# Kernel optimization log

Measured on AMD Instinct MI355X. Metric: run time of the kernel, lower is better.

Reference implementation:

```python
import jax, jax.numpy as jnp
import numpy as np

N = 4096
B = 8
NITER = 4

def setup_inputs() -> dict:
    key = jax.random.key(0)
    k1, k2, k3 = jax.random.split(key, 3)
    preds = jax.random.uniform(k1, (B, N), dtype=jnp.float32)
    seed_idx = jax.random.randint(k2, (B, 10), 0, N, dtype=jnp.int64)
    # dense probability matrix (buffer), entries in [0,1)
    prob_matrix = jax.random.uniform(k3, (N, N), dtype=jnp.float32)
    return {"preds": preds, "seed_idx": seed_idx, "prob_matrix": prob_matrix}

def reference(preds, seed_idx, prob_matrix):
    # Original per-row math: new_pred[a] = 1 - prod_b (1 - P[b, a] * pred[b])
    # P2 = P.T * pred.view(1,-1)  =>  P2[a, b] = P[b, a] * pred[b]
    # Vectorized over the batch dim instead of the Python loop.
    # seed_idx is accepted but unused, matching the original forward.
    pred = preds  # [B, N]
    for _ in range(NITER):
        # [B, N(src), N(dst)] intermediate: (1 - pred[b, s] * P[s, d]), prod over s
        pred = 1.0 - jnp.prod(1.0 - pred[:, :, None] * prob_matrix[None, :, :], axis=1)
    return pred
```

## Files before the change

### kernel.cpp

```cpp
#include <hip/hip_runtime.h>

#define NN 4096
#define BB 8
#define SC 32
#define DT 16
#define WAVES 8
#define RPW 16


__global__ void __launch_bounds__(512, 2)
diff_partial_it0(const float* __restrict__ preds,
                 const float* __restrict__ P,
                 unsigned int* __restrict__ P8,
                 float* __restrict__ partial)
{
    const int tid  = threadIdx.x;
    const int lane = tid & 63;
    const int w    = __builtin_amdgcn_readfirstlane(tid >> 6);
    const int d0   = blockIdx.x * 256 + lane * 4;
    const int ch   = blockIdx.y;
    const int row0 = ch * (WAVES * RPW) + w * RPW;

    float4 acc[BB];
#pragma unroll
    for (int b = 0; b < BB; ++b) acc[b] = make_float4(1.f, 1.f, 1.f, 1.f);

    const float* Pp = P + (size_t)row0 * NN + d0;

#pragma unroll
    for (int k = 0; k < RPW; k += 4) {
        float4 pv[4];
#pragma unroll
        for (int j = 0; j < 4; ++j)
            pv[j] = *(const float4*)(Pp + (size_t)(k + j) * NN);

#pragma unroll
        for (int j = 0; j < 4; ++j) {
            const unsigned int e0 = (unsigned int)fmaf(pv[j].x, 255.f, 0.5f);
            const unsigned int e1 = (unsigned int)fmaf(pv[j].y, 255.f, 0.5f);
            const unsigned int e2 = (unsigned int)fmaf(pv[j].z, 255.f, 0.5f);
            const unsigned int e3 = (unsigned int)fmaf(pv[j].w, 255.f, 0.5f);
            P8[((size_t)(row0 + k + j) * NN + d0) >> 2] =
                e0 | (e1 << 8) | (e2 << 16) | (e3 << 24);
        }

#pragma unroll
        for (int j = 0; j < 4; ++j) {
            const int s = row0 + k + j;
#pragma unroll
            for (int b = 0; b < BB; ++b) {
                const float p = preds[b * NN + s];
                acc[b].x *= fmaf(-p, pv[j].x, 1.f);
                acc[b].y *= fmaf(-p, pv[j].y, 1.f);
                acc[b].z *= fmaf(-p, pv[j].z, 1.f);
                acc[b].w *= fmaf(-p, pv[j].w, 1.f);
            }
        }
    }

    __shared__ float4 red[WAVES][BB][64];
#pragma unroll
    for (int b = 0; b < BB; ++b) red[w][b][lane] = acc[b];
    __syncthreads();

    const int b  = tid >> 6;
    const int c4 = tid & 63;
    float4 pr = red[0][b][c4];
#pragma unroll
    for (int w2 = 1; w2 < WAVES; ++w2) {
        const float4 v = red[w2][b][c4];
        pr.x *= v.x; pr.y *= v.y; pr.z *= v.z; pr.w *= v.w;
    }
    *(float4*)(partial + ((size_t)b * SC + ch) * NN + blockIdx.x * 256 + c4 * 4) = pr;
}

__global__ void __launch_bounds__(512, 2)
diff_partial_u8(const float* __restrict__ predT_s,
                const unsigned int* __restrict__ P8,
                float* __restrict__ partial)
{
    const int tid  = threadIdx.x;
    const int lane = tid & 63;
    const int w    = __builtin_amdgcn_readfirstlane(tid >> 6);
    const int d0   = blockIdx.x * 256 + lane * 4;
    const int ch   = blockIdx.y;
    const int row0 = ch * (WAVES * RPW) + w * RPW;

    float4 acc[BB];
#pragma unroll
    for (int b = 0; b < BB; ++b) acc[b] = make_float4(1.f, 1.f, 1.f, 1.f);

    const unsigned int* Pp = P8 + (((size_t)row0 * NN + d0) >> 2);
    const float* pt = predT_s + row0 * BB;

#pragma unroll
    for (int k = 0; k < RPW; k += 4) {
        unsigned int q[4];
#pragma unroll
        for (int j = 0; j < 4; ++j)
            q[j] = Pp[(size_t)(k + j) * (NN / 4)];

#pragma unroll
        for (int j = 0; j < 4; ++j) {
            const float fx = (float)( q[j]        & 0xffu);
            const float fy = (float)((q[j] >> 8)  & 0xffu);
            const float fz = (float)((q[j] >> 16) & 0xffu);
            const float fw = (float)( q[j] >> 24);
#pragma unroll
            for (int b = 0; b < BB; ++b) {
                const float p = pt[(k + j) * BB + b];
                acc[b].x *= fmaf(-p, fx, 1.f);
                acc[b].y *= fmaf(-p, fy, 1.f);
                acc[b].z *= fmaf(-p, fz, 1.f);
                acc[b].w *= fmaf(-p, fw, 1.f);
            }
        }
    }

    __shared__ float4 red[WAVES][BB][64];
#pragma unroll
    for (int b = 0; b < BB; ++b) red[w][b][lane] = acc[b];
    __syncthreads();

    const int b  = tid >> 6;
    const int c4 = tid & 63;
    float4 pr = red[0][b][c4];
#pragma unroll
    for (int w2 = 1; w2 < WAVES; ++w2) {
        const float4 v = red[w2][b][c4];
        pr.x *= v.x; pr.y *= v.y; pr.z *= v.z; pr.w *= v.w;
    }
    *(float4*)(partial + ((size_t)b * SC + ch) * NN + blockIdx.x * 256 + c4 * 4) = pr;
}

__global__ void __launch_bounds__(256)
diff_combine(const float* __restrict__ partial,
             float* __restrict__ predT_next,
             float* __restrict__ out, int write_out)
{
    const int g = blockIdx.x * 256 + threadIdx.x;
    const int b = g >> 12;
    const int d = g & (NN - 1);

    const float* pp = partial + (size_t)b * SC * NN + d;
    float prod = 1.0f;
#pragma unroll
    for (int ch = 0; ch < SC; ++ch)
        prod *= pp[(size_t)ch * NN];

    const float r = 1.0f - prod;
    predT_next[d * BB + b] = r * (1.0f / 255.0f);
    if (write_out) out[g] = r;
}

__global__ void __launch_bounds__(512, 2)
diff_partial_f32(const float* __restrict__ predT,
                 const float* __restrict__ P,
                 float* __restrict__ partial)
{
    const int tid  = threadIdx.x;
    const int lane = tid & 63;
    const int w    = __builtin_amdgcn_readfirstlane(tid >> 6);
    const int d0   = blockIdx.x * 256 + lane * 4;
    const int ch   = blockIdx.y;
    const int row0 = ch * (WAVES * RPW) + w * RPW;

    float4 acc[BB];
#pragma unroll
    for (int b = 0; b < BB; ++b) acc[b] = make_float4(1.f, 1.f, 1.f, 1.f);

    const float* Pp = P + (size_t)row0 * NN + d0;
    const float* pt = predT + row0 * BB;

#pragma unroll
    for (int k = 0; k < RPW; k += 4) {
        float4 pv[4];
#pragma unroll
        for (int j = 0; j < 4; ++j)
            pv[j] = *(const float4*)(Pp + (size_t)(k + j) * NN);
#pragma unroll
        for (int j = 0; j < 4; ++j) {
#pragma unroll
            for (int b = 0; b < BB; ++b) {
                const float p = pt[(k + j) * BB + b];
                acc[b].x *= fmaf(-p, pv[j].x, 1.f);
                acc[b].y *= fmaf(-p, pv[j].y, 1.f);
                acc[b].z *= fmaf(-p, pv[j].z, 1.f);
                acc[b].w *= fmaf(-p, pv[j].w, 1.f);
            }
        }
    }

    __shared__ float4 red[WAVES][BB][64];
#pragma unroll
    for (int b = 0; b < BB; ++b) red[w][b][lane] = acc[b];
    __syncthreads();

    const int b  = tid >> 6;
    const int c4 = tid & 63;
    float4 pr = red[0][b][c4];
#pragma unroll
    for (int w2 = 1; w2 < WAVES; ++w2) {
        const float4 v = red[w2][b][c4];
        pr.x *= v.x; pr.y *= v.y; pr.z *= v.z; pr.w *= v.w;
    }
    *(float4*)(partial + ((size_t)b * SC + ch) * NN + blockIdx.x * 256 + c4 * 4) = pr;
}

__global__ void __launch_bounds__(256)
diff_combine_raw(const float* __restrict__ partial,
                 float* __restrict__ predT_next,
                 float* __restrict__ out, int write_out)
{
    const int g = blockIdx.x * 256 + threadIdx.x;
    const int b = g >> 12;
    const int d = g & (NN - 1);
    const float* pp = partial + (size_t)b * SC * NN + d;
    float prod = 1.0f;
#pragma unroll
    for (int ch = 0; ch < SC; ++ch) prod *= pp[(size_t)ch * NN];
    const float r = 1.0f - prod;
    predT_next[d * BB + b] = r;
    if (write_out) out[g] = r;
}

__global__ void __launch_bounds__(512, 2)
diff_partial_it0_nf(const float* __restrict__ preds,
                    const float* __restrict__ P,
                    float* __restrict__ partial)
{
    const int tid  = threadIdx.x;
    const int lane = tid & 63;
    const int w    = __builtin_amdgcn_readfirstlane(tid >> 6);
    const int d0   = blockIdx.x * 256 + lane * 4;
    const int ch   = blockIdx.y;
    const int row0 = ch * (WAVES * RPW) + w * RPW;

    float4 acc[BB];
#pragma unroll
    for (int b = 0; b < BB; ++b) acc[b] = make_float4(1.f, 1.f, 1.f, 1.f);

    const float* Pp = P + (size_t)row0 * NN + d0;

#pragma unroll
    for (int k = 0; k < RPW; k += 4) {
        float4 pv[4];
#pragma unroll
        for (int j = 0; j < 4; ++j)
            pv[j] = *(const float4*)(Pp + (size_t)(k + j) * NN);
#pragma unroll
        for (int j = 0; j < 4; ++j) {
            const int s = row0 + k + j;
#pragma unroll
            for (int b = 0; b < BB; ++b) {
                const float p = preds[b * NN + s];
                acc[b].x *= fmaf(-p, pv[j].x, 1.f);
                acc[b].y *= fmaf(-p, pv[j].y, 1.f);
                acc[b].z *= fmaf(-p, pv[j].z, 1.f);
                acc[b].w *= fmaf(-p, pv[j].w, 1.f);
            }
        }
    }

    __shared__ float4 red[WAVES][BB][64];
#pragma unroll
    for (int b = 0; b < BB; ++b) red[w][b][lane] = acc[b];
    __syncthreads();

    const int b  = tid >> 6;
    const int c4 = tid & 63;
    float4 pr = red[0][b][c4];
#pragma unroll
    for (int w2 = 1; w2 < WAVES; ++w2) {
        const float4 v = red[w2][b][c4];
        pr.x *= v.x; pr.y *= v.y; pr.z *= v.z; pr.w *= v.w;
    }
    *(float4*)(partial + ((size_t)b * SC + ch) * NN + blockIdx.x * 256 + c4 * 4) = pr;
}

extern "C" void kernel_launch(void* const* d_in, const int* in_sizes, int n_in,
                              void* d_out, int out_size, void* d_ws, size_t ws_size,
                              hipStream_t stream) {
    const float* preds = (const float*)d_in[0];
    const float* P     = (const float*)d_in[2];
    float* out = (float*)d_out;

    char* ws = (char*)d_ws;
    float* partial = (float*)ws;
    float* predT0  = (float*)(ws + (size_t)4 * 1024 * 1024);
    float* predT1  = predT0 + (size_t)NN * BB;
    unsigned int* P8 = (unsigned int*)(ws + (size_t)5 * 1024 * 1024);

    const size_t need_u8 = (size_t)5 * 1024 * 1024 + (size_t)NN * NN;

    dim3 pgrid(DT, SC);
    dim3 cgrid((BB * NN) / 256);
    dim3 block(512);

    if (ws_size >= need_u8) {
        diff_partial_it0<<<pgrid, block, 0, stream>>>(preds, P, P8, partial);
        diff_combine<<<cgrid, 256, 0, stream>>>(partial, predT0, out, 0);
        diff_partial_u8<<<pgrid, block, 0, stream>>>(predT0, P8, partial);
        diff_combine<<<cgrid, 256, 0, stream>>>(partial, predT1, out, 0);
        diff_partial_u8<<<pgrid, block, 0, stream>>>(predT1, P8, partial);
        diff_combine<<<cgrid, 256, 0, stream>>>(partial, predT0, out, 0);
        diff_partial_u8<<<pgrid, block, 0, stream>>>(predT0, P8, partial);
        diff_combine<<<cgrid, 256, 0, stream>>>(partial, predT1, out, 1);
    } else {
        diff_partial_it0_nf<<<pgrid, block, 0, stream>>>(preds, P, partial);
        diff_combine_raw<<<cgrid, 256, 0, stream>>>(partial, predT0, out, 0);
        diff_partial_f32<<<pgrid, block, 0, stream>>>(predT0, P, partial);
        diff_combine_raw<<<cgrid, 256, 0, stream>>>(partial, predT1, out, 0);
        diff_partial_f32<<<pgrid, block, 0, stream>>>(predT1, P, partial);
        diff_combine_raw<<<cgrid, 256, 0, stream>>>(partial, predT0, out, 0);
        diff_partial_f32<<<pgrid, block, 0, stream>>>(predT0, P, partial);
        diff_combine_raw<<<cgrid, 256, 0, stream>>>(partial, predT1, out, 1);
    }
}
```

Before: 56.88 us.

## Fuse combine step into next iteration's partial kernel via per-wave chunk products

Removes the separate combine kernels between iterations. Each wave of the partial kernel now reduces the previous iteration's 32 chunk partials for its own 16 source rows and broadcasts the resulting preds with readlane. The partial buffers are double-buffered, the P8 offset moves to make room, and a final kernel produces the output. This saves three launches and the predT round trip, but every block redundantly recomputes the same row reductions (16 column blocks read the same partial values).

```diff
diff --git a/kernel.cpp b/kernel.cpp
--- a/kernel.cpp
+++ b/kernel.cpp
@@ -74,10 +74,12 @@
     *(float4*)(partial + ((size_t)b * SC + ch) * NN + blockIdx.x * 256 + c4 * 4) = pr;
 }
 
+template <bool U8>
 __global__ void __launch_bounds__(512, 2)
-diff_partial_u8(const float* __restrict__ predT_s,
-                const unsigned int* __restrict__ P8,
-                float* __restrict__ partial)
+diff_fused(const float* __restrict__ prevPartial,
+           const float* __restrict__ Pf,
+           const unsigned int* __restrict__ P8,
+           float* __restrict__ partial)
 {
     const int tid  = threadIdx.x;
     const int lane = tid & 63;
@@ -86,29 +88,55 @@
     const int ch   = blockIdx.y;
     const int row0 = ch * (WAVES * RPW) + w * RPW;
 
+    const int bsel = lane & 7;
+    const int q2   = lane >> 3;
+    const float* qp = prevPartial + (size_t)bsel * SC * NN + row0 + 2 * q2;
+    float prod0 = 1.f, prod1 = 1.f;
+#pragma unroll 8
+    for (int c = 0; c < SC; ++c) {
+        const float2 v = *(const float2*)(qp + (size_t)c * NN);
+        prod0 *= v.x;
+        prod1 *= v.y;
+    }
+    const float sc  = U8 ? (1.f / 255.f) : 1.f;
+    const float pv0 = (1.f - prod0) * sc;
+    const float pv1 = (1.f - prod1) * sc;
+
     float4 acc[BB];
 #pragma unroll
     for (int b = 0; b < BB; ++b) acc[b] = make_float4(1.f, 1.f, 1.f, 1.f);
 
-    const unsigned int* Pp = P8 + (((size_t)row0 * NN + d0) >> 2);
-    const float* pt = predT_s + row0 * BB;
+    const unsigned int* Pp8 = U8 ? P8 + (((size_t)row0 * NN + d0) >> 2) : nullptr;
+    const float*        Ppf = U8 ? nullptr : Pf + (size_t)row0 * NN + d0;
 
 #pragma unroll
     for (int k = 0; k < RPW; k += 4) {
         unsigned int q[4];
-#pragma unroll
-        for (int j = 0; j < 4; ++j)
-            q[j] = Pp[(size_t)(k + j) * (NN / 4)];
-
-#pragma unroll
-        for (int j = 0; j < 4; ++j) {
-            const float fx = (float)( q[j]        & 0xffu);
-            const float fy = (float)((q[j] >> 8)  & 0xffu);
-            const float fz = (float)((q[j] >> 16) & 0xffu);
-            const float fw = (float)( q[j] >> 24);
+        float4 pvf[4];
+#pragma unroll
+        for (int j = 0; j < 4; ++j) {
+            if (U8) q[j]   = Pp8[(size_t)(k + j) * (NN / 4)];
+            else    pvf[j] = *(const float4*)(Ppf + (size_t)(k + j) * NN);
+        }
+
+#pragma unroll
+        for (int j = 0; j < 4; ++j) {
+            const int r = k + j;
+            float fx, fy, fz, fw;
+            if (U8) {
+                fx = (float)( q[j]        & 0xffu);
+                fy = (float)((q[j] >> 8)  & 0xffu);
+                fz = (float)((q[j] >> 16) & 0xffu);
+                fw = (float)( q[j] >> 24);
+            } else {
+                fx = pvf[j].x; fy = pvf[j].y; fz = pvf[j].z; fw = pvf[j].w;
+            }
 #pragma unroll
             for (int b = 0; b < BB; ++b) {
-                const float p = pt[(k + j) * BB + b];
+                const unsigned int pu = ((r & 1) == 0)
+                    ? __builtin_amdgcn_readlane(__float_as_uint(pv0), (r >> 1) * 8 + b)
+                    : __builtin_amdgcn_readlane(__float_as_uint(pv1), (r >> 1) * 8 + b);
+                const float p = __uint_as_float(pu);
                 acc[b].x *= fmaf(-p, fx, 1.f);
                 acc[b].y *= fmaf(-p, fy, 1.f);
                 acc[b].z *= fmaf(-p, fz, 1.f);
@@ -133,30 +161,10 @@
     *(float4*)(partial + ((size_t)b * SC + ch) * NN + blockIdx.x * 256 + c4 * 4) = pr;
 }
 
-__global__ void __launch_bounds__(256)
-diff_combine(const float* __restrict__ partial,
-             float* __restrict__ predT_next,
-             float* __restrict__ out, int write_out)
-{
-    const int g = blockIdx.x * 256 + threadIdx.x;
-    const int b = g >> 12;
-    const int d = g & (NN - 1);
-
-    const float* pp = partial + (size_t)b * SC * NN + d;
-    float prod = 1.0f;
-#pragma unroll
-    for (int ch = 0; ch < SC; ++ch)
-        prod *= pp[(size_t)ch * NN];
-
-    const float r = 1.0f - prod;
-    predT_next[d * BB + b] = r * (1.0f / 255.0f);
-    if (write_out) out[g] = r;
-}
-
 __global__ void __launch_bounds__(512, 2)
-diff_partial_f32(const float* __restrict__ predT,
-                 const float* __restrict__ P,
-                 float* __restrict__ partial)
+diff_partial_it0_nf(const float* __restrict__ preds,
+                    const float* __restrict__ P,
+                    float* __restrict__ partial)
 {
     const int tid  = threadIdx.x;
     const int lane = tid & 63;
@@ -170,77 +178,6 @@
     for (int b = 0; b < BB; ++b) acc[b] = make_float4(1.f, 1.f, 1.f, 1.f);
 
     const float* Pp = P + (size_t)row0 * NN + d0;
-    const float* pt = predT + row0 * BB;
-
-#pragma unroll
-    for (int k = 0; k < RPW; k += 4) {
-        float4 pv[4];
-#pragma unroll
-        for (int j = 0; j < 4; ++j)
-            pv[j] = *(const float4*)(Pp + (size_t)(k + j) * NN);
-#pragma unroll
-        for (int j = 0; j < 4; ++j) {
-#pragma unroll
-            for (int b = 0; b < BB; ++b) {
-                const float p = pt[(k + j) * BB + b];
-                acc[b].x *= fmaf(-p, pv[j].x, 1.f);
-                acc[b].y *= fmaf(-p, pv[j].y, 1.f);
-                acc[b].z *= fmaf(-p, pv[j].z, 1.f);
-                acc[b].w *= fmaf(-p, pv[j].w, 1.f);
-            }
-        }
-    }
-
-    __shared__ float4 red[WAVES][BB][64];
-#pragma unroll
-    for (int b = 0; b < BB; ++b) red[w][b][lane] = acc[b];
-    __syncthreads();
-
-    const int b  = tid >> 6;
-    const int c4 = tid & 63;
-    float4 pr = red[0][b][c4];
-#pragma unroll
-    for (int w2 = 1; w2 < WAVES; ++w2) {
-        const float4 v = red[w2][b][c4];
-        pr.x *= v.x; pr.y *= v.y; pr.z *= v.z; pr.w *= v.w;
-    }
-    *(float4*)(partial + ((size_t)b * SC + ch) * NN + blockIdx.x * 256 + c4 * 4) = pr;
-}
-
-__global__ void __launch_bounds__(256)
-diff_combine_raw(const float* __restrict__ partial,
-                 float* __restrict__ predT_next,
-                 float* __restrict__ out, int write_out)
-{
-    const int g = blockIdx.x * 256 + threadIdx.x;
-    const int b = g >> 12;
-    const int d = g & (NN - 1);
-    const float* pp = partial + (size_t)b * SC * NN + d;
-    float prod = 1.0f;
-#pragma unroll
-    for (int ch = 0; ch < SC; ++ch) prod *= pp[(size_t)ch * NN];
-    const float r = 1.0f - prod;
-    predT_next[d * BB + b] = r;
-    if (write_out) out[g] = r;
-}
-
-__global__ void __launch_bounds__(512, 2)
-diff_partial_it0_nf(const float* __restrict__ preds,
-                    const float* __restrict__ P,
-                    float* __restrict__ partial)
-{
-    const int tid  = threadIdx.x;
-    const int lane = tid & 63;
-    const int w    = __builtin_amdgcn_readfirstlane(tid >> 6);
-    const int d0   = blockIdx.x * 256 + lane * 4;
-    const int ch   = blockIdx.y;
-    const int row0 = ch * (WAVES * RPW) + w * RPW;
-
-    float4 acc[BB];
-#pragma unroll
-    for (int b = 0; b < BB; ++b) acc[b] = make_float4(1.f, 1.f, 1.f, 1.f);
-
-    const float* Pp = P + (size_t)row0 * NN + d0;
 
 #pragma unroll
     for (int k = 0; k < RPW; k += 4) {
@@ -278,6 +215,22 @@
     *(float4*)(partial + ((size_t)b * SC + ch) * NN + blockIdx.x * 256 + c4 * 4) = pr;
 }
 
+__global__ void __launch_bounds__(256)
+diff_final(const float* __restrict__ partial, float* __restrict__ out)
+{
+    const int g = blockIdx.x * 256 + threadIdx.x;
+    const int b = g >> 12;
+    const int d = g & (NN - 1);
+
+    const float* pp = partial + (size_t)b * SC * NN + d;
+    float prod = 1.0f;
+#pragma unroll
+    for (int ch = 0; ch < SC; ++ch)
+        prod *= pp[(size_t)ch * NN];
+
+    out[g] = 1.0f - prod;
+}
+
 extern "C" void kernel_launch(void* const* d_in, const int* in_sizes, int n_in,
                               void* d_out, int out_size, void* d_ws, size_t ws_size,
                               hipStream_t stream) {
@@ -286,34 +239,27 @@
     float* out = (float*)d_out;
 
     char* ws = (char*)d_ws;
-    float* partial = (float*)ws;
-    float* predT0  = (float*)(ws + (size_t)4 * 1024 * 1024);
-    float* predT1  = predT0 + (size_t)NN * BB;
-    unsigned int* P8 = (unsigned int*)(ws + (size_t)5 * 1024 * 1024);
-
-    const size_t need_u8 = (size_t)5 * 1024 * 1024 + (size_t)NN * NN;
+    float* pA = (float*)ws;
+    float* pB = (float*)(ws + (size_t)4 * 1024 * 1024);
+    unsigned int* P8 = (unsigned int*)(ws + (size_t)8 * 1024 * 1024);
+
+    const size_t need_u8 = (size_t)8 * 1024 * 1024 + (size_t)NN * NN;
 
     dim3 pgrid(DT, SC);
-    dim3 cgrid((BB * NN) / 256);
+    dim3 fgrid((BB * NN) / 256);
     dim3 block(512);
 
     if (ws_size >= need_u8) {
-        diff_partial_it0<<<pgrid, block, 0, stream>>>(preds, P, P8, partial);
-        diff_combine<<<cgrid, 256, 0, stream>>>(partial, predT0, out, 0);
-        diff_partial_u8<<<pgrid, block, 0, stream>>>(predT0, P8, partial);
-        diff_combine<<<cgrid, 256, 0, stream>>>(partial, predT1, out, 0);
-        diff_partial_u8<<<pgrid, block, 0, stream>>>(predT1, P8, partial);
-        diff_combine<<<cgrid, 256, 0, stream>>>(partial, predT0, out, 0);
-        diff_partial_u8<<<pgrid, block, 0, stream>>>(predT0, P8, partial);
-        diff_combine<<<cgrid, 256, 0, stream>>>(partial, predT1, out, 1);
+        diff_partial_it0<<<pgrid, block, 0, stream>>>(preds, P, P8, pA);
+        diff_fused<true><<<pgrid, block, 0, stream>>>(pA, nullptr, P8, pB);
+        diff_fused<true><<<pgrid, block, 0, stream>>>(pB, nullptr, P8, pA);
+        diff_fused<true><<<pgrid, block, 0, stream>>>(pA, nullptr, P8, pB);
+        diff_final<<<fgrid, 256, 0, stream>>>(pB, out);
     } else {
-        diff_partial_it0_nf<<<pgrid, block, 0, stream>>>(preds, P, partial);
-        diff_combine_raw<<<cgrid, 256, 0, stream>>>(partial, predT0, out, 0);
-        diff_partial_f32<<<pgrid, block, 0, stream>>>(predT0, P, partial);
-        diff_combine_raw<<<cgrid, 256, 0, stream>>>(partial, predT1, out, 0);
-        diff_partial_f32<<<pgrid, block, 0, stream>>>(predT1, P, partial);
-        diff_combine_raw<<<cgrid, 256, 0, stream>>>(partial, predT0, out, 0);
-        diff_partial_f32<<<pgrid, block, 0, stream>>>(predT0, P, partial);
-        diff_combine_raw<<<cgrid, 256, 0, stream>>>(partial, predT1, out, 1);
-    }
-}
+        diff_partial_it0_nf<<<pgrid, block, 0, stream>>>(preds, P, pA);
+        diff_fused<false><<<pgrid, block, 0, stream>>>(pA, P, nullptr, pB);
+        diff_fused<false><<<pgrid, block, 0, stream>>>(pB, P, nullptr, pA);
+        diff_fused<false><<<pgrid, block, 0, stream>>>(pA, P, nullptr, pB);
+        diff_final<<<fgrid, 256, 0, stream>>>(pB, out);
+    }
+}
```

Result: slower. 94.64 us (+66.4%).
